# Performance work log

Measured on AMD Instinct MI355X. Metric: run time of the kernel, lower is better.

## Reference

```python
import jax, jax.numpy as jnp
import numpy as np

NEG_INF = -1.0e9
LEAKY_SLOPE = 0.2


def setup_inputs() -> dict:
    key = jax.random.key(0)
    ks = jax.random.split(key, 8)
    B, H, N, D = 4, 8, 256, 64
    query = jax.random.normal(ks[0], (B, H, N, D), dtype=jnp.float32)
    k_ = jax.random.normal(ks[1], (B, H, N, D), dtype=jnp.float32)
    value = jax.random.normal(ks[2], (B, H, N, D), dtype=jnp.float32)
    mask = jax.random.randint(ks[3], (B, 1, N, N), 0, 2, dtype=jnp.int32)
    # nn.Linear(d_k*2, d_k): weight (D, 2D), bias (D,)
    lim_h = 1.0 / np.sqrt(2 * D)
    W_h = jax.random.uniform(ks[4], (D, 2 * D), minval=-lim_h, maxval=lim_h, dtype=jnp.float32)
    b_h = jax.random.uniform(ks[5], (D,), minval=-lim_h, maxval=lim_h, dtype=jnp.float32)
    # nn.Linear(d_k, 1): weight (1, D), bias (1,)
    lim_o = 1.0 / np.sqrt(D)
    W_o = jax.random.uniform(ks[6], (1, D), minval=-lim_o, maxval=lim_o, dtype=jnp.float32)
    b_o = jax.random.uniform(ks[7], (1,), minval=-lim_o, maxval=lim_o, dtype=jnp.float32)
    return {"query": query, "key": k_, "value": value, "mask": mask,
            "W_h": W_h, "b_h": b_h, "W_o": W_o, "b_o": b_o}


def reference(query, key, value, mask, W_h, b_h, W_o, b_o):
    # W_h acts on concat([q, k]); decompose into two projections (same math):
    # W_h @ [q; k] = q @ W_q^T + k @ W_k^T
    D = query.shape[-1]
    Wq, Wk = W_h[:, :D], W_h[:, D:]
    q_proj = jnp.einsum('bhnd,ed->bhne', query, Wq)  # (B,H,N,D)
    k_proj = jnp.einsum('bhmd,ed->bhme', key, Wk)    # (B,H,N,D)
    # pairwise hidden: (B,H,N,N,D)
    hidden = q_proj[:, :, :, None, :] + k_proj[:, :, None, :, :] + b_h
    hidden = jax.nn.leaky_relu(hidden, negative_slope=LEAKY_SLOPE)
    scores = jnp.einsum('bhnme,e->bhnm', hidden, W_o[0]) + b_o[0]  # (B,H,N,N)
    scores = jnp.where(mask == 0, NEG_INF, scores)
    p_attn = jax.nn.softmax(scores, axis=-1)
    out = jnp.einsum('bhnm,bhmd->bhnd', p_attn, value)
    return out, p_attn
```

## Files before the change

### kernel.cpp

```cpp
#include <hip/hip_runtime.h>

typedef float v2f __attribute__((ext_vector_type(2)));

constexpr int B = 4, H = 8, N = 256, D = 64;
constexpr int QBLK = 8;
constexpr int PATTN_OFF = B * H * N * D;
constexpr int NROWS = B * H * N;


__global__ __launch_bounds__(256) void proj_kernel(
    const float* __restrict__ q, const float* __restrict__ k,
    const float* __restrict__ W_h, const float* __restrict__ b_h,
    const float* __restrict__ W_o, const float* __restrict__ b_o,
    float* __restrict__ qp, float* __restrict__ kpb,
    float* __restrict__ cq6, float* __restrict__ ck6, float* __restrict__ w4)
{
    __shared__ float WT[128 * 65];
    int t = threadIdx.x;
    int lane = t & 63;
    int wid = __builtin_amdgcn_readfirstlane(t >> 6);
    int bid = blockIdx.x;
    int work = (bid & 7) * 32 + (bid >> 3);

    #pragma unroll
    for (int i = 0; i < 8; ++i) {
        int fidx = (t + i * 256) * 4;
        float4 w = *reinterpret_cast<const float4*>(W_h + fidx);
        int e = fidx >> 7, d = fidx & 127;
        WT[(d + 0) * 65 + e] = w.x;
        WT[(d + 1) * 65 + e] = w.y;
        WT[(d + 2) * 65 + e] = w.z;
        WT[(d + 3) * 65 + e] = w.w;
    }
    if (bid == 0 && t < 64) w4[t] = 0.4f * W_o[t];
    __syncthreads();

    int rbase = work * 32 + wid * 8;
    float accq[8] = {}, acck[8] = {};
    #pragma unroll
    for (int d0 = 0; d0 < 64; d0 += 16) {
        float wq[16], wk[16];
        #pragma unroll
        for (int d = 0; d < 16; ++d) {
            wq[d] = WT[(d0 + d) * 65 + lane];
            wk[d] = WT[(64 + d0 + d) * 65 + lane];
        }
        #pragma unroll
        for (int j = 0; j < 8; ++j) {
            const float* qrow = q + (rbase + j) * 64 + d0;
            const float* krow = k + (rbase + j) * 64 + d0;
            #pragma unroll
            for (int d = 0; d < 16; ++d) {
                accq[j] = fmaf(qrow[d], wq[d], accq[j]);
                acck[j] = fmaf(krow[d], wk[d], acck[j]);
            }
        }
    }
    float bh_e = b_h[lane];
    float wo = W_o[lane];
    float bo = b_o[0];
    #pragma unroll
    for (int j = 0; j < 8; ++j) {
        float aq = accq[j];
        float ak = acck[j] + bh_e;
        qp[(rbase + j) * 64 + lane] = aq;
        kpb[(rbase + j) * 64 + lane] = ak;
        float sq = wo * aq, sk = wo * ak;
        #pragma unroll
        for (int off = 32; off > 0; off >>= 1) {
            sq += __shfl_xor(sq, off, 64);
            sk += __shfl_xor(sk, off, 64);
        }
        if (lane == 0) {
            cq6[rbase + j] = 0.6f * sq + bo;
            ck6[rbase + j] = 0.6f * sk;
        }
    }
}

__global__ __launch_bounds__(512, 2) void attn_kernel(
    const float* __restrict__ qp, const float* __restrict__ kpb,
    const float* __restrict__ V, const int* __restrict__ mask,
    const float* __restrict__ cq6, const float* __restrict__ ck6,
    const float* __restrict__ w4g,
    float* __restrict__ out)
{
    __shared__ float smem[6144];
    __shared__ float red_s[8][4];

    int t = threadIdx.x;
    int lane = t & 63;
    int wid = __builtin_amdgcn_readfirstlane(t >> 6);
    int h = wid >> 2;
    int m = t & 255;
    int bid = blockIdx.x;
    int work = (bid & 7) * 128 + (bid >> 3);
    int bh = work >> 5;
    int nb = work & 31;
    int b = bh >> 3;
    int n0 = nb * QBLK;
    int kvbase = bh * N * 64;

    const float4* kp4 = reinterpret_cast<const float4*>(kpb + kvbase + m * 64 + h * 32);
    float4 c0 = kp4[0], c1 = kp4[1];

    float mf[4];
    #pragma unroll
    for (int i = 0; i < 4; ++i)
        mf[i] = (mask[(b * N + n0 + h * 4 + i) * N + m] != 0) ? 1.0f : 0.0f;

    float ckt = (h == 0) ? ck6[bh * N + m] : 0.f;

    v2f sp2[8];
    const float* cq = cq6 + bh * N + n0;
    #pragma unroll
    for (int r = 0; r < 8; ++r) {
        float init = (h == 0) ? (cq[r] + ckt) : 0.f;
        sp2[r] = (v2f){init, 0.f};
    }

    const v2f* qr2 = reinterpret_cast<const v2f*>(qp + (bh * N + n0) * 64 + h * 32);
    const v2f* w42 = reinterpret_cast<const v2f*>(w4g + h * 32);
    #pragma unroll
    for (int chunk = 0; chunk < 4; ++chunk) {
        float4 pf0, pf1;
        if (chunk < 3) { pf0 = kp4[2 * chunk + 2]; pf1 = kp4[2 * chunk + 3]; }
        v2f kp2[4] = {{c0.x, c0.y}, {c0.z, c0.w}, {c1.x, c1.y}, {c1.z, c1.w}};
        #pragma unroll
        for (int p = 0; p < 4; ++p) {
            v2f w2 = w42[chunk * 4 + p];
            v2f k2 = kp2[p];
            #pragma unroll
            for (int r = 0; r < 8; ++r) {
                v2f x = qr2[r * 32 + chunk * 4 + p] + k2;
                v2f ax = __builtin_elementwise_max(x, -x);
                sp2[r] = __builtin_elementwise_fma(w2, ax, sp2[r]);
            }
        }
        c0 = pf0; c1 = pf1;
    }
    #pragma unroll
    for (int r = 0; r < 8; ++r)
        smem[h * 2048 + r * 256 + m] = sp2[r].x + sp2[r].y;

    const float* Vp = V + kvbase + wid * 32 * 64 + lane;
    float vpre0 = Vp[0 * 64], vpre1 = Vp[1 * 64], vpre2 = Vp[2 * 64], vpre3 = Vp[3 * 64];
    __syncthreads();

    float p8[4];
    #pragma unroll
    for (int i = 0; i < 4; ++i) {
        int rr = h * 4 + i;
        float s = smem[rr * 256 + m] + smem[2048 + rr * 256 + m];
        float p = __expf(s) * mf[i];
        p8[i] = p;
        float l = p;
        #pragma unroll
        for (int off = 32; off > 0; off >>= 1) l += __shfl_xor(l, off, 64);
        if (lane == 0) red_s[wid][i] = l;
    }
    __syncthreads();

    #pragma unroll
    for (int i = 0; i < 4; ++i) {
        int rr = h * 4 + i;
        float gs = red_s[h*4+0][i] + red_s[h*4+1][i] + red_s[h*4+2][i] + red_s[h*4+3][i];
        float pn = p8[i] * __frcp_rn(gs);
        smem[rr * 256 + m] = pn;
        out[PATTN_OFF + (bh * N + n0 + rr) * N + m] = pn;
    }
    __syncthreads();

    v2f acc2[8] = {};
    {
        v2f va = {vpre0, vpre1}, vb = {vpre2, vpre3};
        #pragma unroll
        for (int r = 0; r < 8; ++r) {
            float4 p4 = *reinterpret_cast<const float4*>(&smem[r * 256 + wid * 32]);
            v2f pa = {p4.x, p4.y}, pb = {p4.z, p4.w};
            acc2[r] = __builtin_elementwise_fma(pa, va, acc2[r]);
            acc2[r] = __builtin_elementwise_fma(pb, vb, acc2[r]);
        }
    }
    #pragma unroll
    for (int j = 4; j < 32; j += 4) {
        v2f va = {Vp[(j+0) * 64], Vp[(j+1) * 64]};
        v2f vb = {Vp[(j+2) * 64], Vp[(j+3) * 64]};
        #pragma unroll
        for (int r = 0; r < 8; ++r) {
            float4 p4 = *reinterpret_cast<const float4*>(&smem[r * 256 + wid * 32 + j]);
            v2f pa = {p4.x, p4.y}, pb = {p4.z, p4.w};
            acc2[r] = __builtin_elementwise_fma(pa, va, acc2[r]);
            acc2[r] = __builtin_elementwise_fma(pb, vb, acc2[r]);
        }
    }
    #pragma unroll
    for (int r = 0; r < 8; ++r)
        smem[2048 + wid * 512 + r * 64 + lane] = acc2[r].x + acc2[r].y;
    __syncthreads();

    float o = 0.f;
    #pragma unroll
    for (int mc = 0; mc < 8; ++mc)
        o += smem[2048 + mc * 512 + wid * 64 + lane];
    out[(bh * N + n0 + wid) * 64 + lane] = o;
}

extern "C" void kernel_launch(void* const* d_in, const int* in_sizes, int n_in,
                              void* d_out, int out_size, void* d_ws, size_t ws_size,
                              hipStream_t stream) {
    const float* q    = (const float*)d_in[0];
    const float* k    = (const float*)d_in[1];
    const float* v    = (const float*)d_in[2];
    const int*   mask = (const int*)d_in[3];
    const float* W_h  = (const float*)d_in[4];
    const float* b_h  = (const float*)d_in[5];
    const float* W_o  = (const float*)d_in[6];
    const float* b_o  = (const float*)d_in[7];
    float* out = (float*)d_out;

    float* qp  = (float*)d_ws;
    float* kpb = qp + NROWS * 64;
    float* cq6 = kpb + NROWS * 64;
    float* ck6 = cq6 + NROWS;
    float* w4  = ck6 + NROWS;

    proj_kernel<<<NROWS / 32, 256, 0, stream>>>(q, k, W_h, b_h, W_o, b_o, qp, kpb, cq6, ck6, w4);
    attn_kernel<<<B * H * (N / QBLK), 512, 0, stream>>>(qp, kpb, v, mask, cq6, ck6, w4, out);
}
```

Baseline: 39.72 us.

## Store softmax probs as fp16 in LDS and double proj kernel grid

The normalized attention probabilities are now staged in shared memory as fp16 instead of fp32. This cuts LDS footprint and read traffic for the P·V product, which now loads 8 halves per vector read and uses scalar FMAs with 8 prefetched V values. The projection kernel processes 4 rows per wave instead of 8, doubling its grid, and adds an occupancy hint. Rounding P to fp16 slightly reduces output precision, and an extra barrier was added before the scratch buffer is reused.

```diff
diff --git a/kernel.cpp b/kernel.cpp
--- a/kernel.cpp
+++ b/kernel.cpp
@@ -1,6 +1,7 @@
 #include <hip/hip_runtime.h>
 
 typedef float v2f __attribute__((ext_vector_type(2)));
+typedef _Float16 h8 __attribute__((ext_vector_type(8)));
 
 constexpr int B = 4, H = 8, N = 256, D = 64;
 constexpr int QBLK = 8;
@@ -8,7 +9,7 @@
 constexpr int NROWS = B * H * N;
 
 
-__global__ __launch_bounds__(256) void proj_kernel(
+__global__ __launch_bounds__(256, 2) void proj_kernel(
     const float* __restrict__ q, const float* __restrict__ k,
     const float* __restrict__ W_h, const float* __restrict__ b_h,
     const float* __restrict__ W_o, const float* __restrict__ b_o,
@@ -20,7 +21,7 @@
     int lane = t & 63;
     int wid = __builtin_amdgcn_readfirstlane(t >> 6);
     int bid = blockIdx.x;
-    int work = (bid & 7) * 32 + (bid >> 3);
+    int work = (bid & 7) * 64 + (bid >> 3);
 
     #pragma unroll
     for (int i = 0; i < 8; ++i) {
@@ -35,8 +36,8 @@
     if (bid == 0 && t < 64) w4[t] = 0.4f * W_o[t];
     __syncthreads();
 
-    int rbase = work * 32 + wid * 8;
-    float accq[8] = {}, acck[8] = {};
+    int rbase = work * 16 + wid * 4;
+    float accq[4] = {}, acck[4] = {};
     #pragma unroll
     for (int d0 = 0; d0 < 64; d0 += 16) {
         float wq[16], wk[16];
@@ -46,7 +47,7 @@
             wk[d] = WT[(64 + d0 + d) * 65 + lane];
         }
         #pragma unroll
-        for (int j = 0; j < 8; ++j) {
+        for (int j = 0; j < 4; ++j) {
             const float* qrow = q + (rbase + j) * 64 + d0;
             const float* krow = k + (rbase + j) * 64 + d0;
             #pragma unroll
@@ -60,7 +61,7 @@
     float wo = W_o[lane];
     float bo = b_o[0];
     #pragma unroll
-    for (int j = 0; j < 8; ++j) {
+    for (int j = 0; j < 4; ++j) {
         float aq = accq[j];
         float ak = acck[j] + bh_e;
         qp[(rbase + j) * 64 + lane] = aq;
@@ -85,7 +86,8 @@
     const float* __restrict__ w4g,
     float* __restrict__ out)
 {
-    __shared__ float smem[6144];
+    __shared__ float sc[4096];
+    __shared__ _Float16 pf[2048];
     __shared__ float red_s[8][4];
 
     int t = threadIdx.x;
@@ -141,17 +143,19 @@
     }
     #pragma unroll
     for (int r = 0; r < 8; ++r)
-        smem[h * 2048 + r * 256 + m] = sp2[r].x + sp2[r].y;
+        sc[h * 2048 + r * 256 + m] = sp2[r].x + sp2[r].y;
 
     const float* Vp = V + kvbase + wid * 32 * 64 + lane;
-    float vpre0 = Vp[0 * 64], vpre1 = Vp[1 * 64], vpre2 = Vp[2 * 64], vpre3 = Vp[3 * 64];
+    float vpre[8];
+    #pragma unroll
+    for (int g = 0; g < 8; ++g) vpre[g] = Vp[g * 64];
     __syncthreads();
 
     float p8[4];
     #pragma unroll
     for (int i = 0; i < 4; ++i) {
         int rr = h * 4 + i;
-        float s = smem[rr * 256 + m] + smem[2048 + rr * 256 + m];
+        float s = sc[rr * 256 + m] + sc[2048 + rr * 256 + m];
         float p = __expf(s) * mf[i];
         p8[i] = p;
         float l = p;
@@ -166,43 +170,45 @@
         int rr = h * 4 + i;
         float gs = red_s[h*4+0][i] + red_s[h*4+1][i] + red_s[h*4+2][i] + red_s[h*4+3][i];
         float pn = p8[i] * __frcp_rn(gs);
-        smem[rr * 256 + m] = pn;
+        pf[rr * 256 + m] = (_Float16)pn;
         out[PATTN_OFF + (bh * N + n0 + rr) * N + m] = pn;
     }
     __syncthreads();
 
-    v2f acc2[8] = {};
+    float acc[8] = {};
     {
-        v2f va = {vpre0, vpre1}, vb = {vpre2, vpre3};
         #pragma unroll
         for (int r = 0; r < 8; ++r) {
-            float4 p4 = *reinterpret_cast<const float4*>(&smem[r * 256 + wid * 32]);
-            v2f pa = {p4.x, p4.y}, pb = {p4.z, p4.w};
-            acc2[r] = __builtin_elementwise_fma(pa, va, acc2[r]);
-            acc2[r] = __builtin_elementwise_fma(pb, vb, acc2[r]);
-        }
-    }
-    #pragma unroll
-    for (int j = 4; j < 32; j += 4) {
-        v2f va = {Vp[(j+0) * 64], Vp[(j+1) * 64]};
-        v2f vb = {Vp[(j+2) * 64], Vp[(j+3) * 64]};
+            h8 ph = *reinterpret_cast<const h8*>(&pf[r * 256 + wid * 32]);
+            #pragma unroll
+            for (int g = 0; g < 8; ++g)
+                acc[r] = fmaf((float)ph[g], vpre[g], acc[r]);
+        }
+    }
+    #pragma unroll
+    for (int j = 8; j < 32; j += 8) {
+        float vv[8];
+        #pragma unroll
+        for (int g = 0; g < 8; ++g) vv[g] = Vp[(j + g) * 64];
         #pragma unroll
         for (int r = 0; r < 8; ++r) {
-            float4 p4 = *reinterpret_cast<const float4*>(&smem[r * 256 + wid * 32 + j]);
-            v2f pa = {p4.x, p4.y}, pb = {p4.z, p4.w};
-            acc2[r] = __builtin_elementwise_fma(pa, va, acc2[r]);
-            acc2[r] = __builtin_elementwise_fma(pb, vb, acc2[r]);
-        }
-    }
+            h8 ph = *reinterpret_cast<const h8*>(&pf[r * 256 + wid * 32 + j]);
+            #pragma unroll
+            for (int g = 0; g < 8; ++g)
+                acc[r] = fmaf((float)ph[g], vv[g], acc[r]);
+        }
+    }
+    __syncthreads();
+
     #pragma unroll
     for (int r = 0; r < 8; ++r)
-        smem[2048 + wid * 512 + r * 64 + lane] = acc2[r].x + acc2[r].y;
+        sc[wid * 512 + r * 64 + lane] = acc[r];
     __syncthreads();
 
     float o = 0.f;
     #pragma unroll
     for (int mc = 0; mc < 8; ++mc)
-        o += smem[2048 + mc * 512 + wid * 64 + lane];
+        o += sc[mc * 512 + wid * 64 + lane];
     out[(bh * N + n0 + wid) * 64 + lane] = o;
 }
 
@@ -225,6 +231,6 @@
     float* ck6 = cq6 + NROWS;
     float* w4  = ck6 + NROWS;
 
-    proj_kernel<<<NROWS / 32, 256, 0, stream>>>(q, k, W_h, b_h, W_o, b_o, qp, kpb, cq6, ck6, w4);
+    proj_kernel<<<NROWS / 16, 256, 0, stream>>>(q, k, W_h, b_h, W_o, b_o, qp, kpb, cq6, ck6, w4);
     attn_kernel<<<B * H * (N / QBLK), 512, 0, stream>>>(qp, kpb, v, mask, cq6, ck6, w4, out);
 }
```

After: 35.54 us. 1.12x faster.
